# Optimization experiments

Measured on AMD Instinct MI355X. Metric: run time of the kernel, lower is better.

## Reference

```python
import jax, jax.numpy as jnp
import numpy as np


def _unpack_int4(packed):
    """Unpack int8 [O, K//2] -> fp16 [O, K]; each byte holds (high, low) signed nibbles."""
    # Arithmetic right shift on int8 reproduces torch's signed high-nibble extraction.
    high = packed >> 4                                  # [-8, 7]
    low = (packed & jnp.int8(15)).astype(jnp.int8)      # [0, 15]
    low = (low - jnp.int8(16) * (low > 7).astype(jnp.int8)).astype(jnp.int8)
    u = jnp.stack([high, low], axis=-1)                 # [O, K//2, 2]
    u = u.reshape(packed.shape[:-1] + (-1,))            # [O, K]
    return u.astype(jnp.float16)


def setup_inputs() -> dict:
    key = jax.random.key(0)
    k1, k2, k3 = jax.random.split(key, 3)
    B, S, K, O = 4, 2048, 4096, 4096
    x = jax.random.normal(k1, (B, S, K), dtype=jnp.float16)
    weight_int4 = jax.random.randint(k2, (O, K // 2), -128, 128, dtype=jnp.int32).astype(jnp.int8)
    weight_scale = jnp.asarray(0.05, dtype=jnp.float16)  # max_abs/7 style per-tensor scale
    bias = (jax.random.normal(k3, (O,), dtype=jnp.float16) * jnp.float16(0.01))
    return {"x": x, "weight_int4": weight_int4, "weight_scale": weight_scale, "bias": bias}


def reference(x, weight_int4, weight_scale, bias):
    # quantized-path forward: dequantize packed INT4 weights, then F.linear
    W = _unpack_int4(weight_int4) * weight_scale        # [O, K] fp16
    out = jnp.einsum('bsk,ok->bso', x, W)               # [B, S, O]
    return out + bias
```

## Files before the change

kernel.cpp:

```cpp
#include <hip/hip_runtime.h>
#include <hip/hip_bf16.h>
#include <stdint.h>


typedef __bf16 bf16;
typedef __bf16 bf16x8 __attribute__((ext_vector_type(8)));
typedef float  f32x4  __attribute__((ext_vector_type(4)));

constexpr int M_DIM = 8192;
constexpr int N_DIM = 4096;
constexpr int K_DIM = 4096;
constexpr int KB    = K_DIM / 2;

constexpr int BM = 256;
constexpr int BN = 256;
constexpr int BK = 64;
constexpr int NKT = K_DIM / BK;

__device__ __forceinline__ void gload_lds16(const void* g, void* l) {
  __builtin_amdgcn_global_load_lds(
      (const __attribute__((address_space(1))) void*)g,
      (__attribute__((address_space(3))) void*)l,
      16, 0, 0);
}

__device__ __forceinline__ void fence_barrier() {
  asm volatile("" ::: "memory");
  __builtin_amdgcn_s_barrier();
  asm volatile("" ::: "memory");
}

__device__ __forceinline__ float dq_hi_f(int b) {
  int sb = (int)(signed char)(b & 0xFF);
  return (float)(sb >> 4);
}
__device__ __forceinline__ float dq_lo_f(int b) {
  int sb = (int)(signed char)(b & 0xFF);
  return (float)(((sb & 15) ^ 8) - 8);
}

__global__ void convert_x(const float* __restrict__ x, bf16* __restrict__ xc) {
  const size_t i = (size_t)blockIdx.x * 256 + threadIdx.x;
  const float4 a = ((const float4*)x)[2 * i];
  const float4 b = ((const float4*)x)[2 * i + 1];
  bf16x8 o;
  o[0] = (bf16)a.x; o[1] = (bf16)a.y; o[2] = (bf16)a.z; o[3] = (bf16)a.w;
  o[4] = (bf16)b.x; o[5] = (bf16)b.y; o[6] = (bf16)b.z; o[7] = (bf16)b.w;
  *(bf16x8*)(xc + i * 8) = o;
}

__global__ void dequant_w(const int* __restrict__ wq, bf16* __restrict__ W,
                          const float* __restrict__ scale_p) {
  const float s = scale_p[0];
  const size_t idx = (size_t)blockIdx.x * 256 + threadIdx.x;
  const int4 v = ((const int4*)wq)[idx];
  bf16x8 o;
  o[0] = (bf16)(dq_hi_f(v.x) * s); o[1] = (bf16)(dq_lo_f(v.x) * s);
  o[2] = (bf16)(dq_hi_f(v.y) * s); o[3] = (bf16)(dq_lo_f(v.y) * s);
  o[4] = (bf16)(dq_hi_f(v.z) * s); o[5] = (bf16)(dq_lo_f(v.z) * s);
  o[6] = (bf16)(dq_hi_f(v.w) * s); o[7] = (bf16)(dq_lo_f(v.w) * s);
  *(bf16x8*)(W + idx * 8) = o;
}


#define MMA16(AF, BF, ACCOFF)                                                  \
  {                                                                            \
    _Pragma("unroll") for (int i_ = 0; i_ < 4; ++i_) {                         \
      _Pragma("unroll") for (int j_ = 0; j_ < 4; ++j_) {                       \
        acc[(ACCOFF) + i_][j_] = __builtin_amdgcn_mfma_f32_16x16x32_bf16(      \
            (AF)[i_], (BF)[j_], acc[(ACCOFF) + i_][j_], 0, 0, 0);              \
      }                                                                        \
    }                                                                          \
  }

__global__ void __launch_bounds__(512, 2)
gemm8p(const bf16* __restrict__ Xc, const bf16* __restrict__ W,
       const float* __restrict__ bias, float* __restrict__ out) {
  __shared__ __align__(16) bf16 As[2][BM][BK];
  __shared__ __align__(16) bf16 Bs[2][BN][BK];

  const int tid = threadIdx.x;
  const int w   = tid >> 6;
  const int l   = tid & 63;
  const int wm  = w >> 2;
  const int wn  = w & 3;
  const int lrow = l & 15, lg = l >> 4;

  const int bid = blockIdx.x;
  const int wg  = (bid & 7) * 64 + (bid >> 3);
  const int m0  = (wg >> 4) * BM;
  const int n0  = (wg & 15) * BN;

  const int srow = l >> 3;
  const int scol = ((l & 7) ^ srow) << 3;
  const bf16* gA = Xc + (size_t)(m0 + w * 16 + srow) * K_DIM + scol;
  const bf16* gB = W  + (size_t)(n0 + w * 16 + srow) * K_DIM + scol;

  const int rsw = (lrow & 7) << 3;

  f32x4 acc[8][4] = {};

#define STAGE_A(KT, H)                                                         \
  {                                                                            \
    gload_lds16(gA + (size_t)((H) * 128) * K_DIM + (KT) * BK,                  \
                &As[(KT) & 1][(H) * 128 + w * 16][0]);                         \
    gload_lds16(gA + (size_t)((H) * 128 + 8) * K_DIM + (KT) * BK,              \
                &As[(KT) & 1][(H) * 128 + w * 16 + 8][0]);                     \
  }
#define STAGE_B(KT, H)                                                         \
  {                                                                            \
    gload_lds16(gB + (size_t)((H) * 128) * K_DIM + (KT) * BK,                  \
                &Bs[(KT) & 1][(H) * 128 + w * 16][0]);                         \
    gload_lds16(gB + (size_t)((H) * 128 + 8) * K_DIM + (KT) * BK,              \
                &Bs[(KT) & 1][(H) * 128 + w * 16 + 8][0]);                     \
  }

  STAGE_A(0, 0); STAGE_A(0, 1); STAGE_B(0, 0); STAGE_B(0, 1);
  STAGE_A(1, 0); STAGE_A(1, 1);
  asm volatile("s_waitcnt vmcnt(4)" ::: "memory");
  fence_barrier();

  for (int kt = 0; kt < NKT; ++kt) {
    const int buf = kt & 1;
    bf16x8 a0[8], a1[8], b0[4], b1[4];

    if (kt + 1 < NKT) STAGE_B(kt + 1, 0);
#pragma unroll
    for (int i = 0; i < 8; ++i)
      a0[i] = *(const bf16x8*)&As[buf][wm * 128 + i * 16 + lrow][(lg * 8) ^ rsw];
#pragma unroll
    for (int j = 0; j < 4; ++j)
      b0[j] = *(const bf16x8*)&Bs[buf][wn * 64 + j * 16 + lrow][(lg * 8) ^ rsw];
    fence_barrier();
    asm volatile("s_waitcnt lgkmcnt(0)" ::: "memory");
    __builtin_amdgcn_s_setprio(1);
    MMA16(a0, b0, 0);
    __builtin_amdgcn_s_setprio(0);
    fence_barrier();

    if (kt + 1 < NKT) STAGE_B(kt + 1, 1);
#pragma unroll
    for (int i = 0; i < 8; ++i)
      a1[i] = *(const bf16x8*)&As[buf][wm * 128 + i * 16 + lrow][(32 + lg * 8) ^ rsw];
#pragma unroll
    for (int j = 0; j < 4; ++j)
      b1[j] = *(const bf16x8*)&Bs[buf][wn * 64 + j * 16 + lrow][(32 + lg * 8) ^ rsw];
    fence_barrier();
    asm volatile("s_waitcnt lgkmcnt(0)" ::: "memory");
    __builtin_amdgcn_s_setprio(1);
    MMA16(a0 + 4, b0, 4);
    __builtin_amdgcn_s_setprio(0);
    fence_barrier();

    if (kt + 2 < NKT) STAGE_A(kt + 2, 0);
    fence_barrier();
    __builtin_amdgcn_s_setprio(1);
    MMA16(a1, b1, 0);
    __builtin_amdgcn_s_setprio(0);
    fence_barrier();

    if (kt + 2 < NKT) STAGE_A(kt + 2, 1);
    __builtin_amdgcn_s_setprio(1);
    MMA16(a1 + 4, b1, 4);
    __builtin_amdgcn_s_setprio(0);
    if (kt + 2 < NKT) {
      asm volatile("s_waitcnt vmcnt(4)" ::: "memory");
    } else {
      asm volatile("s_waitcnt vmcnt(0)" ::: "memory");
    }
    fence_barrier();
  }

  float bv[4];
#pragma unroll
  for (int j = 0; j < 4; ++j) bv[j] = bias[n0 + wn * 64 + j * 16 + lrow];

#pragma unroll
  for (int i = 0; i < 8; ++i) {
#pragma unroll
    for (int r = 0; r < 4; ++r) {
      float* orow = out + (size_t)(m0 + wm * 128 + i * 16 + lg * 4 + r) * N_DIM
                        + (n0 + wn * 64 + lrow);
#pragma unroll
      for (int j = 0; j < 4; ++j) orow[j * 16] = acc[i][j][r] + bv[j];
    }
  }
}

__global__ void __launch_bounds__(256)
gemm_fused(const float* __restrict__ Xf, const int* __restrict__ WQ,
           const float* __restrict__ scale_p, const float* __restrict__ bias,
           float* __restrict__ out) {
  __shared__ __align__(16) bf16 As[128][64];
  __shared__ __align__(16) bf16 Bs[128][64];
  const int tid = threadIdx.x;
  const int w = tid >> 6, l = tid & 63;
  const int nwg = gridDim.x, cpx = nwg >> 3, bid = blockIdx.x;
  const int wg = (bid & 7) * cpx + (bid >> 3);
  const int ntN = N_DIM / 128;
  const int m0 = (wg / ntN) * 128, n0 = (wg % ntN) * 128;
  const int wm = w >> 1, wn = w & 1;
  const int lrow = l & 15, lg = l >> 4;
  f32x4 acc[4][4] = {};
  const float s = scale_p[0];
  const int rr = tid >> 1, rh = tid & 1;
  for (int k0 = 0; k0 < K_DIM; k0 += 64) {
    const float* gx = Xf + (size_t)(m0 + rr) * K_DIM + k0 + rh * 32;
    float4 xa[8];
#pragma unroll
    for (int u = 0; u < 8; ++u) xa[u] = ((const float4*)gx)[u];
    bf16* dst = &As[rr][rh * 32];
#pragma unroll
    for (int u = 0; u < 4; ++u) {
      const float4 p = xa[2 * u], q = xa[2 * u + 1];
      bf16x8 o;
      o[0] = (bf16)p.x; o[1] = (bf16)p.y; o[2] = (bf16)p.z; o[3] = (bf16)p.w;
      o[4] = (bf16)q.x; o[5] = (bf16)q.y; o[6] = (bf16)q.z; o[7] = (bf16)q.w;
      *(bf16x8*)(dst + u * 8) = o;
    }
    const int4* gq = (const int4*)(WQ + (size_t)(n0 + rr) * KB + (k0 >> 1) + rh * 16);
    const int4 q0 = gq[0], q1 = gq[1], q2 = gq[2], q3 = gq[3];
    const int vals[16] = {q0.x, q0.y, q0.z, q0.w, q1.x, q1.y, q1.z, q1.w,
                          q2.x, q2.y, q2.z, q2.w, q3.x, q3.y, q3.z, q3.w};
    bf16* bdst = &Bs[rr][rh * 32];
#pragma unroll
    for (int u = 0; u < 4; ++u) {
      bf16x8 ov;
#pragma unroll
      for (int e = 0; e < 4; ++e) {
        const int b = vals[u * 4 + e];
        ov[e * 2]     = (bf16)(dq_hi_f(b) * s);
        ov[e * 2 + 1] = (bf16)(dq_lo_f(b) * s);
      }
      *(bf16x8*)(bdst + u * 8) = ov;
    }
    __syncthreads();
#pragma unroll
    for (int kk = 0; kk < 64; kk += 32) {
      bf16x8 af[4], bfr[4];
#pragma unroll
      for (int i = 0; i < 4; ++i)
        af[i] = *(const bf16x8*)&As[wm * 64 + i * 16 + lrow][kk + lg * 8];
#pragma unroll
      for (int j = 0; j < 4; ++j)
        bfr[j] = *(const bf16x8*)&Bs[wn * 64 + j * 16 + lrow][kk + lg * 8];
#pragma unroll
      for (int i = 0; i < 4; ++i)
#pragma unroll
        for (int j = 0; j < 4; ++j)
          acc[i][j] = __builtin_amdgcn_mfma_f32_16x16x32_bf16(af[i], bfr[j],
                                                              acc[i][j], 0, 0, 0);
    }
    __syncthreads();
  }
  float bv[4];
#pragma unroll
  for (int j = 0; j < 4; ++j) bv[j] = bias[n0 + wn * 64 + j * 16 + lrow];
#pragma unroll
  for (int i = 0; i < 4; ++i)
#pragma unroll
    for (int r = 0; r < 4; ++r) {
      float* orow = out + (size_t)(m0 + wm * 64 + i * 16 + lg * 4 + r) * N_DIM
                        + (n0 + wn * 64 + lrow);
#pragma unroll
      for (int j = 0; j < 4; ++j) orow[j * 16] = acc[i][j][r] + bv[j];
    }
}

extern "C" void kernel_launch(void* const* d_in, const int* in_sizes, int n_in,
                              void* d_out, int out_size, void* d_ws, size_t ws_size,
                              hipStream_t stream) {
  const float* x     = (const float*)d_in[0];
  const int*   wq    = (const int*)d_in[1];
  const float* scale = (const float*)d_in[2];
  const float* bias  = (const float*)d_in[3];
  float*       out   = (float*)d_out;

  const size_t wb = (size_t)N_DIM * K_DIM * sizeof(bf16);
  const size_t xb = (size_t)M_DIM * K_DIM * sizeof(bf16);

  if (ws_size >= wb + xb) {
    bf16* Wd = (bf16*)d_ws;
    bf16* Xc = (bf16*)((char*)d_ws + wb);
    dequant_w<<<(N_DIM * KB / 4) / 256, 256, 0, stream>>>(wq, Wd, scale);
    convert_x<<<((size_t)M_DIM * K_DIM / 8) / 256, 256, 0, stream>>>(x, Xc);
    gemm8p<<<dim3((M_DIM / BM) * (N_DIM / BN)), 512, 0, stream>>>(Xc, Wd, bias, out);
  } else {
    gemm_fused<<<dim3((M_DIM / 128) * (N_DIM / 128)), 256, 0, stream>>>(
        x, wq, scale, bias, out);
  }
}
```

Measured before the change: 533.8 us.

## Software-pipeline LDS fragment reads across K tiles with register double buffering

Restructures the main loop to unroll by two tiles. It keeps two register sets for the first K-slice fragments, so the next tile's slice-0 LDS reads are issued while the current tile's last MMA group runs. Each tile's B loads are issued together, and the number of barriers per tile drops from about six to two. In exchange it uses more VGPRs for the extra fragment buffers and waits with vmcnt(0) instead of vmcnt(4), which may expose global-load latency.

```diff
diff --git a/kernel.cpp b/kernel.cpp
--- a/kernel.cpp
+++ b/kernel.cpp
@@ -115,60 +115,57 @@
                 &Bs[(KT) & 1][(H) * 128 + w * 16 + 8][0]);                     \
   }
 
+#define READ_KS0(BUF, AD, BD)                                                  \
+  {                                                                            \
+    _Pragma("unroll") for (int i_ = 0; i_ < 8; ++i_)                           \
+      AD[i_] = *(const bf16x8*)&As[BUF][wm * 128 + i_ * 16 + lrow][(lg * 8) ^ rsw]; \
+    _Pragma("unroll") for (int j_ = 0; j_ < 4; ++j_)                           \
+      BD[j_] = *(const bf16x8*)&Bs[BUF][wn * 64 + j_ * 16 + lrow][(lg * 8) ^ rsw];  \
+  }
+#define READ_KS1(BUF, AD, BD)                                                  \
+  {                                                                            \
+    _Pragma("unroll") for (int i_ = 0; i_ < 8; ++i_)                           \
+      AD[i_] = *(const bf16x8*)&As[BUF][wm * 128 + i_ * 16 + lrow][(32 + lg * 8) ^ rsw]; \
+    _Pragma("unroll") for (int j_ = 0; j_ < 4; ++j_)                           \
+      BD[j_] = *(const bf16x8*)&Bs[BUF][wn * 64 + j_ * 16 + lrow][(32 + lg * 8) ^ rsw]; \
+  }
+
+  bf16x8 a0A[8], a0B[8], a1[8];
+  bf16x8 b0A[4], b0B[4], b1[4];
+
   STAGE_A(0, 0); STAGE_A(0, 1); STAGE_B(0, 0); STAGE_B(0, 1);
   STAGE_A(1, 0); STAGE_A(1, 1);
   asm volatile("s_waitcnt vmcnt(4)" ::: "memory");
   fence_barrier();
-
-  for (int kt = 0; kt < NKT; ++kt) {
-    const int buf = kt & 1;
-    bf16x8 a0[8], a1[8], b0[4], b1[4];
-
-    if (kt + 1 < NKT) STAGE_B(kt + 1, 0);
-#pragma unroll
-    for (int i = 0; i < 8; ++i)
-      a0[i] = *(const bf16x8*)&As[buf][wm * 128 + i * 16 + lrow][(lg * 8) ^ rsw];
-#pragma unroll
-    for (int j = 0; j < 4; ++j)
-      b0[j] = *(const bf16x8*)&Bs[buf][wn * 64 + j * 16 + lrow][(lg * 8) ^ rsw];
-    fence_barrier();
-    asm volatile("s_waitcnt lgkmcnt(0)" ::: "memory");
-    __builtin_amdgcn_s_setprio(1);
-    MMA16(a0, b0, 0);
-    __builtin_amdgcn_s_setprio(0);
-    fence_barrier();
-
-    if (kt + 1 < NKT) STAGE_B(kt + 1, 1);
-#pragma unroll
-    for (int i = 0; i < 8; ++i)
-      a1[i] = *(const bf16x8*)&As[buf][wm * 128 + i * 16 + lrow][(32 + lg * 8) ^ rsw];
-#pragma unroll
-    for (int j = 0; j < 4; ++j)
-      b1[j] = *(const bf16x8*)&Bs[buf][wn * 64 + j * 16 + lrow][(32 + lg * 8) ^ rsw];
-    fence_barrier();
-    asm volatile("s_waitcnt lgkmcnt(0)" ::: "memory");
-    __builtin_amdgcn_s_setprio(1);
-    MMA16(a0 + 4, b0, 4);
-    __builtin_amdgcn_s_setprio(0);
-    fence_barrier();
-
-    if (kt + 2 < NKT) STAGE_A(kt + 2, 0);
-    fence_barrier();
-    __builtin_amdgcn_s_setprio(1);
-    MMA16(a1, b1, 0);
-    __builtin_amdgcn_s_setprio(0);
-    fence_barrier();
-
-    if (kt + 2 < NKT) STAGE_A(kt + 2, 1);
-    __builtin_amdgcn_s_setprio(1);
-    MMA16(a1 + 4, b1, 4);
-    __builtin_amdgcn_s_setprio(0);
-    if (kt + 2 < NKT) {
-      asm volatile("s_waitcnt vmcnt(4)" ::: "memory");
-    } else {
-      asm volatile("s_waitcnt vmcnt(0)" ::: "memory");
-    }
-    fence_barrier();
+  READ_KS0(0, a0A, b0A);
+
+#define TILE(KT, BUF, A0C, B0C, A0N, B0N)                                      \
+  {                                                                            \
+                                                                       \
+    if ((KT) + 1 < NKT) { STAGE_B((KT) + 1, 0); STAGE_B((KT) + 1, 1); }        \
+    READ_KS1(BUF, a1, b1);                                                     \
+    __builtin_amdgcn_s_setprio(1);                                             \
+    MMA16(A0C, B0C, 0);                                                        \
+                                                                       \
+    MMA16(A0C + 4, B0C, 4);                                                    \
+                                                                       \
+    MMA16(a1, b1, 0);                                                          \
+    __builtin_amdgcn_s_setprio(0);                                             \
+    asm volatile("s_waitcnt lgkmcnt(0)" ::: "memory");                         \
+    asm volatile("s_waitcnt vmcnt(0)" ::: "memory");                           \
+    fence_barrier();                                                           \
+                                                                       \
+    if ((KT) + 2 < NKT) { STAGE_A((KT) + 2, 0); STAGE_A((KT) + 2, 1); }        \
+    if ((KT) + 1 < NKT) { READ_KS0((BUF) ^ 1, A0N, B0N); }                     \
+    __builtin_amdgcn_s_setprio(1);                                             \
+    MMA16(a1 + 4, b1, 4);                                                      \
+    __builtin_amdgcn_s_setprio(0);                                             \
+    fence_barrier();                                                           \
+  }
+
+  for (int kt = 0; kt < NKT; kt += 2) {
+    TILE(kt,     0, a0A, b0A, a0B, b0B);
+    TILE(kt + 1, 1, a0B, b0B, a0A, b0A);
   }
 
   float bv[4];
```

After: 1.339 ms. 2.51x slower.
